# Kernel tuning notes

Measured on AMD Instinct MI355X. Metric: run time of the kernel, lower is better.

The kernel has to match this reference:

```python
import jax, jax.numpy as jnp
import numpy as np

D_MODEL = 1024
NUM_HEADS = 16
D_K = D_MODEL // NUM_HEADS
THETA = 10000.0
BATCH = 2
SEQ = 2048


def setup_inputs() -> dict:
    key = jax.random.key(0)
    ks = jax.random.split(key, 5)
    std = np.sqrt(2.0 / (D_MODEL + D_MODEL))
    return {
        "x": jax.random.normal(ks[0], (BATCH, SEQ, D_MODEL), dtype=jnp.float32),
        "Wq": jax.random.normal(ks[1], (D_MODEL, D_MODEL), dtype=jnp.float32) * std,
        "Wk": jax.random.normal(ks[2], (D_MODEL, D_MODEL), dtype=jnp.float32) * std,
        "Wv": jax.random.normal(ks[3], (D_MODEL, D_MODEL), dtype=jnp.float32) * std,
        "Wo": jax.random.normal(ks[4], (D_MODEL, D_MODEL), dtype=jnp.float32) * std,
        "token_positions": jnp.arange(SEQ, dtype=jnp.int64),
    }


def _apply_rope(t, cos, sin):
    # t: [B, H, S, D_K]; cos/sin: [S, D_K//2]
    # Block-diag 2x2 rotation on consecutive pairs (2k, 2k+1) == elementwise rotation.
    tr = t.reshape(*t.shape[:-1], D_K // 2, 2)
    t0, t1 = tr[..., 0], tr[..., 1]
    o0 = t0 * cos - t1 * sin
    o1 = t0 * sin + t1 * cos
    return jnp.stack([o0, o1], axis=-1).reshape(t.shape)


def reference(x, Wq, Wk, Wv, Wo, token_positions):
    B, S, _ = x.shape
    # projections: custom Linear does x @ W.T
    def split_heads(t):
        return t.reshape(B, S, NUM_HEADS, D_K).transpose(0, 2, 1, 3)  # [B,H,S,Dk]

    q = split_heads(x @ Wq.T)
    k = split_heads(x @ Wk.T)
    v = split_heads(x @ Wv.T)

    # RoPE angle table: theta_ik = pos / THETA**(2k/d_k)
    inv_freq = 1.0 / (THETA ** (2.0 * jnp.arange(D_K // 2, dtype=jnp.float32) / D_K))
    angles = token_positions.astype(jnp.float32)[:, None] * inv_freq[None, :]  # [S, Dk//2]
    cos, sin = jnp.cos(angles), jnp.sin(angles)

    q = _apply_rope(q, cos, sin)
    k = _apply_rope(k, cos, sin)

    scale = 1.0 / np.sqrt(D_K)
    scores = jnp.einsum("bhqd,bhkd->bhqk", q, k) * scale  # [B,H,S,S]
    causal = jnp.tril(jnp.ones((S, S), dtype=bool))
    scores = jnp.where(causal, scores, -jnp.inf)
    attn = jax.nn.softmax(scores, axis=-1)
    out = jnp.einsum("bhqk,bhkd->bhqd", attn, v)  # [B,H,S,Dk]
    out = out.transpose(0, 2, 1, 3).reshape(B, S, D_MODEL)
    return out @ Wo.T
```

## Files before the change

kernel.cpp:

```cpp
#include <hip/hip_runtime.h>
#include <hip/hip_bf16.h>
#include <cstdint>
#include <cstddef>

#define BATCH 2
#define SEQ   2048
#define DM    1024
#define NH    16
#define DK    64
#define LOG2E 1.4426950408889634f

typedef __attribute__((ext_vector_type(8)))  short short8;
typedef __attribute__((ext_vector_type(4)))  float f32x4;
typedef __attribute__((ext_vector_type(16))) float f32x16;
typedef __attribute__((ext_vector_type(4)))  int   i32x4;
typedef __attribute__((ext_vector_type(2)))  int   i32x2;

__device__ __forceinline__ void gload_lds16(const __hip_bfloat16* g, __hip_bfloat16* l) {
  __builtin_amdgcn_global_load_lds((const __attribute__((address_space(1))) void*)g,
                                   (__attribute__((address_space(3))) void*)l, 16, 0, 0);
}

__device__ __forceinline__ int cvtpk_bf16(float lo, float hi) {
  int r;
  asm("v_cvt_pk_bf16_f32 %0, %1, %2" : "=v"(r) : "v"(lo), "v"(hi));
  return r;
}

__device__ __forceinline__ float bf2f(short v) {
  return __int_as_float(((int)(unsigned short)v) << 16);
}

__device__ __forceinline__ float partner32(float x, int hi) {
  auto r = __builtin_amdgcn_permlane32_swap(__float_as_int(x), __float_as_int(x), false, false);
  return __int_as_float(hi ? r[0] : r[1]);
}

__global__ void cast_all(const float* __restrict__ x,  const float* __restrict__ Wq,
                         const float* __restrict__ Wk, const float* __restrict__ Wv,
                         const float* __restrict__ Wo, __hip_bfloat16* __restrict__ dst,
                         const int* __restrict__ pos,  float2* __restrict__ tbl) {
  const int NX = BATCH * SEQ * DM;
  int t = blockIdx.x * 256 + threadIdx.x;
  if (t < SEQ * 32) {
    int s = t >> 5, d2 = t & 31;
    float ang = (float)pos[s] * exp2f(-(float)d2 * 0.415241011860920f);
    float cv, sv;
    __sincosf(ang, &sv, &cv);
    tbl[t] = make_float2(cv, sv);
  }
  size_t i = (size_t)t * 4;
  const float* s;
  if (i < (size_t)NX) {
    s = x + i;
  } else {
    size_t j = i - NX;
    int wsel = (int)(j >> 20);
    size_t o = j & ((1u << 20) - 1);
    s = (wsel == 0 ? Wq : wsel == 1 ? Wk : wsel == 2 ? Wv : Wo) + o;
  }
  float4 v = *(const float4*)s;
  i32x2 pk;
  pk[0] = cvtpk_bf16(v.x, v.y);
  pk[1] = cvtpk_bf16(v.z, v.w);
  *(i32x2*)(dst + i) = pk;
}

template<bool F32OUT, bool VSPLIT>
__global__ __launch_bounds__(256)
void gemm_bt(const __hip_bfloat16* __restrict__ A,
             const __hip_bfloat16* __restrict__ Bw,
             void* __restrict__ Cv, __hip_bfloat16* __restrict__ vt,
             int M, int N, int K, int ldc) {
  __shared__ __hip_bfloat16 As[2][128 * 32];
  __shared__ __hip_bfloat16 Bs[2][128 * 32];
  const int tid  = threadIdx.x;
  const int lane = tid & 63;
  const int w    = tid >> 6;
  const int wr   = w >> 1, wc = w & 1;
  const int g    = lane >> 4;
  const int lr   = lane & 15;

  const int nwg = gridDim.x * gridDim.y;
  const int bid = blockIdx.y * gridDim.x + blockIdx.x;
  const int cpx = nwg >> 3;
  const int sbid = (bid & 7) * cpx + (bid >> 3);
  const int bx = sbid % gridDim.x, by = sbid / gridDim.x;
  const int bm0  = by * 128;
  const int bn0  = bx * 128;

  f32x4 acc[4][4] = {};

  const int strow = lane >> 2;
  const int stcol = (lane & 3) * 8;

  auto STAGE = [&](int buf, int kt) {
    #pragma unroll
    for (int it = 0; it < 2; ++it) {
      int row = (w * 2 + it) * 16 + strow;
      gload_lds16(A  + (size_t)(bm0 + row) * K + kt + stcol, &As[buf][row * 32 + stcol]);
      gload_lds16(Bw + (size_t)(bn0 + row) * K + kt + stcol, &Bs[buf][row * 32 + stcol]);
    }
  };

  STAGE(0, 0);
  __syncthreads();
  int cur = 0;
  const int nk = K / 32;
  for (int ki = 0; ki < nk; ++ki) {
    if (ki + 1 < nk) STAGE(cur ^ 1, (ki + 1) * 32);
    short8 a[4], b[4];
    #pragma unroll
    for (int m = 0; m < 4; ++m)
      a[m] = *(const short8*)(&As[cur][(wr * 64 + m * 16 + lr) * 32 + g * 8]);
    #pragma unroll
    for (int n = 0; n < 4; ++n)
      b[n] = *(const short8*)(&Bs[cur][(wc * 64 + n * 16 + lr) * 32 + g * 8]);
    #pragma unroll
    for (int m = 0; m < 4; ++m)
      #pragma unroll
      for (int n = 0; n < 4; ++n)
        acc[m][n] = __builtin_amdgcn_mfma_f32_16x16x32_bf16(a[m], b[n], acc[m][n], 0, 0, 0);
    __syncthreads();
    cur ^= 1;
  }

  if (VSPLIT && bn0 >= 2048) {
    #pragma unroll
    for (int m = 0; m < 4; ++m)
      #pragma unroll
      for (int n = 0; n < 4; ++n) {
        int nn = bn0 + wc * 64 + n * 16 + lr - 2048;
        int hd = nn >> 6, d = nn & 63;
        int m0 = bm0 + wr * 64 + m * 16 + g * 4;
        int bb = m0 >> 11, ss = m0 & 2047;
        i32x2 pk;
        pk[0] = cvtpk_bf16(acc[m][n][0], acc[m][n][1]);
        pk[1] = cvtpk_bf16(acc[m][n][2], acc[m][n][3]);
        *(i32x2*)(vt + ((size_t)(bb * NH + hd) * DK + d) * SEQ + ss) = pk;
      }
  } else {
    #pragma unroll
    for (int m = 0; m < 4; ++m)
      #pragma unroll
      for (int n = 0; n < 4; ++n) {
        int col = bn0 + wc * 64 + n * 16 + lr;
        #pragma unroll
        for (int r = 0; r < 4; ++r) {
          int row = bm0 + wr * 64 + m * 16 + g * 4 + r;
          float v = acc[m][n][r];
          if (F32OUT) ((float*)Cv)[(size_t)row * ldc + col] = v;
          else        ((__hip_bfloat16*)Cv)[(size_t)row * ldc + col] = __float2bfloat16(v);
        }
      }
  }
}

__global__ void rope_vec(__hip_bfloat16* __restrict__ qk, const float2* __restrict__ tbl) {
  int idx = blockIdx.x * 256 + threadIdx.x;
  int row = idx >> 7;
  int hg  = idx & 127;
  int h   = hg >> 3, gg = hg & 7;
  const float QS = 0.125f * LOG2E;
  size_t base = (size_t)row * 2048 + h * 64 + gg * 8;
  const float2* tp = tbl + (row & (SEQ - 1)) * 32 + gg * 4;
  short8 q = *(const short8*)(qk + base);
  short8 k = *(const short8*)(qk + base + 1024);
  i32x4 qo, ko;
  #pragma unroll
  for (int j = 0; j < 4; ++j) {
    float2 cs = tp[j];
    float q0 = bf2f(q[2 * j]), q1 = bf2f(q[2 * j + 1]);
    float k0 = bf2f(k[2 * j]), k1 = bf2f(k[2 * j + 1]);
    qo[j] = cvtpk_bf16((q0 * cs.x - q1 * cs.y) * QS, (q0 * cs.y + q1 * cs.x) * QS);
    ko[j] = cvtpk_bf16(k0 * cs.x - k1 * cs.y,        k0 * cs.y + k1 * cs.x);
  }
  *(i32x4*)(qk + base)        = qo;
  *(i32x4*)(qk + base + 1024) = ko;
}

__global__ __launch_bounds__(512)
void flash_attn(const __hip_bfloat16* __restrict__ qk,
                const __hip_bfloat16* __restrict__ vt,
                __hip_bfloat16* __restrict__ outb) {
  __shared__ __hip_bfloat16 Kls[2][2][64 * 64];
  __shared__ __hip_bfloat16 Vls[2][2][64 * 64];
  const int pi = blockIdx.x;
  const int NQB = SEQ / 128;
  const int qbh = NQB - 1 - pi, qbl = pi;
  const int hd = blockIdx.y, b = blockIdx.z;
  const int tid = threadIdx.x, lane = tid & 63, w = tid >> 6;
  const int wh = w & 3;
  const int qb_eff = (w < 4) ? qbh : qbl;
  const int hi = lane >> 5, ql = lane & 31;
  const int q0w = qb_eff * 128 + wh * 32;
  const int nph  = qbh + 1;

  const __hip_bfloat16* Qb = qk + (size_t)(b * SEQ) * 2048 + hd * DK;
  const __hip_bfloat16* Kg = qk + (size_t)(b * SEQ) * 2048 + 1024 + hd * DK;
  const __hip_bfloat16* Vg = vt + (size_t)(b * NH + hd) * DK * SEQ;

  short8 qf[4];
  #pragma unroll
  for (int c = 0; c < 4; ++c)
    qf[c] = *(const short8*)(Qb + (size_t)(q0w + ql) * 2048 + c * 16 + hi * 8);

  f32x16 o0 = {}, o1 = {};
  float l_run = 0.f;

  const int srow = tid >> 3;
  const int sc0  = (tid & 7) * 8;
  const int swz  = (srow & 7) << 3;

  short8 kr0, kr1, vr0, vr1;
  auto LOAD = [&](int ph) {
    int r0 = ph * 128;
    kr0 = *(const short8*)(Kg + (size_t)(r0 + srow) * 2048 + sc0);
    kr1 = *(const short8*)(Kg + (size_t)(r0 + 64 + srow) * 2048 + sc0);
    vr0 = *(const short8*)(Vg + (size_t)srow * SEQ + r0 + sc0);
    vr1 = *(const short8*)(Vg + (size_t)srow * SEQ + r0 + 64 + sc0);
  };
  auto WRITE = [&](int buf) {
    *(short8*)(&Kls[buf][0][srow * 64 + (sc0 ^ swz)]) = kr0;
    *(short8*)(&Kls[buf][1][srow * 64 + (sc0 ^ swz)]) = kr1;
    *(short8*)(&Vls[buf][0][srow * 64 + (sc0 ^ swz)]) = vr0;
    *(short8*)(&Vls[buf][1][srow * 64 + (sc0 ^ swz)]) = vr1;
  };

  LOAD(0);
  WRITE(0);

  for (int ph = 0; ph < nph; ++ph) {
    const int cur = ph & 1;
    if (ph + 1 < nph) LOAD(ph + 1);
    __syncthreads();

    if (ph <= qb_eff) {
      const int t0 = 2 * ph, t1 = 2 * ph + 1;

      f32x16 sA0 = {}, sA1 = {}, sB0 = {}, sB1 = {};
      __builtin_amdgcn_s_setprio(1);
      #pragma unroll
      for (int c = 0; c < 4; ++c) {
        int col = (c * 16 + hi * 8) ^ ((ql & 7) << 3);
        short8 ka = *(const short8*)(&Kls[cur][0][ql * 64 + col]);
        short8 kb = *(const short8*)(&Kls[cur][0][(32 + ql) * 64 + col]);
        short8 kc = *(const short8*)(&Kls[cur][1][ql * 64 + col]);
        short8 kd = *(const short8*)(&Kls[cur][1][(32 + ql) * 64 + col]);
        sA0 = __builtin_amdgcn_mfma_f32_32x32x16_bf16(ka, qf[c], sA0, 0, 0, 0);
        sA1 = __builtin_amdgcn_mfma_f32_32x32x16_bf16(kb, qf[c], sA1, 0, 0, 0);
        sB0 = __builtin_amdgcn_mfma_f32_32x32x16_bf16(kc, qf[c], sB0, 0, 0, 0);
        sB1 = __builtin_amdgcn_mfma_f32_32x32x16_bf16(kd, qf[c], sB1, 0, 0, 0);
      }
      __builtin_amdgcn_s_setprio(0);

      if (t0 * 64 + 63 > q0w) {
        int qg = q0w + ql;
        #pragma unroll
        for (int r = 0; r < 16; ++r) {
          int krow = (r & 3) + 8 * (r >> 2) + 4 * hi;
          if (t0 * 64 + krow > qg)      sA0[r] = -1e30f;
          if (t0 * 64 + 32 + krow > qg) sA1[r] = -1e30f;
        }
      }
      if (t1 * 64 + 63 > q0w) {
        int qg = q0w + ql;
        #pragma unroll
        for (int r = 0; r < 16; ++r) {
          int krow = (r & 3) + 8 * (r >> 2) + 4 * hi;
          if (t1 * 64 + krow > qg)      sB0[r] = -1e30f;
          if (t1 * 64 + 32 + krow > qg) sB1[r] = -1e30f;
        }
      }

      float sum = 0.f;
      #pragma unroll
      for (int r = 0; r < 16; ++r) { sA0[r] = __builtin_amdgcn_exp2f(sA0[r]); sum += sA0[r]; }
      #pragma unroll
      for (int r = 0; r < 16; ++r) { sA1[r] = __builtin_amdgcn_exp2f(sA1[r]); sum += sA1[r]; }
      #pragma unroll
      for (int r = 0; r < 16; ++r) { sB0[r] = __builtin_amdgcn_exp2f(sB0[r]); sum += sB0[r]; }
      #pragma unroll
      for (int r = 0; r < 16; ++r) { sB1[r] = __builtin_amdgcn_exp2f(sB1[r]); sum += sB1[r]; }
      sum += partner32(sum, hi);
      l_run += sum;

      short8 pfA[4], pfB[4];
      #pragma unroll
      for (int kt = 0; kt < 2; ++kt) {
        const f32x16& sv = kt ? sA1 : sA0;
        #pragma unroll
        for (int u = 0; u < 2; ++u) {
          int wa0 = cvtpk_bf16(sv[8 * u + 0], sv[8 * u + 1]);
          int wa1 = cvtpk_bf16(sv[8 * u + 2], sv[8 * u + 3]);
          int wb0 = cvtpk_bf16(sv[8 * u + 4], sv[8 * u + 5]);
          int wb1 = cvtpk_bf16(sv[8 * u + 6], sv[8 * u + 7]);
          auto r0 = __builtin_amdgcn_permlane32_swap(wa0, wb0, false, false);
          auto r1 = __builtin_amdgcn_permlane32_swap(wa1, wb1, false, false);
          i32x4 fr; fr[0] = r0[0]; fr[1] = r1[0]; fr[2] = r0[1]; fr[3] = r1[1];
          pfA[kt * 2 + u] = *(short8*)&fr;
        }
      }
      #pragma unroll
      for (int kt = 0; kt < 2; ++kt) {
        const f32x16& sv = kt ? sB1 : sB0;
        #pragma unroll
        for (int u = 0; u < 2; ++u) {
          int wa0 = cvtpk_bf16(sv[8 * u + 0], sv[8 * u + 1]);
          int wa1 = cvtpk_bf16(sv[8 * u + 2], sv[8 * u + 3]);
          int wb0 = cvtpk_bf16(sv[8 * u + 4], sv[8 * u + 5]);
          int wb1 = cvtpk_bf16(sv[8 * u + 6], sv[8 * u + 7]);
          auto r0 = __builtin_amdgcn_permlane32_swap(wa0, wb0, false, false);
          auto r1 = __builtin_amdgcn_permlane32_swap(wa1, wb1, false, false);
          i32x4 fr; fr[0] = r0[0]; fr[1] = r1[0]; fr[2] = r0[1]; fr[3] = r1[1];
          pfB[kt * 2 + u] = *(short8*)&fr;
        }
      }

      __builtin_amdgcn_s_setprio(1);
      #pragma unroll
      for (int cc = 0; cc < 4; ++cc) {
        int col = (cc * 16 + hi * 8) ^ ((ql & 7) << 3);
        short8 va = *(const short8*)(&Vls[cur][0][ql * 64 + col]);
        short8 vb = *(const short8*)(&Vls[cur][0][(32 + ql) * 64 + col]);
        o0 = __builtin_amdgcn_mfma_f32_32x32x16_bf16(va, pfA[cc], o0, 0, 0, 0);
        o1 = __builtin_amdgcn_mfma_f32_32x32x16_bf16(vb, pfA[cc], o1, 0, 0, 0);
      }
      #pragma unroll
      for (int cc = 0; cc < 4; ++cc) {
        int col = (cc * 16 + hi * 8) ^ ((ql & 7) << 3);
        short8 vc = *(const short8*)(&Vls[cur][1][ql * 64 + col]);
        short8 vd = *(const short8*)(&Vls[cur][1][(32 + ql) * 64 + col]);
        o0 = __builtin_amdgcn_mfma_f32_32x32x16_bf16(vc, pfB[cc], o0, 0, 0, 0);
        o1 = __builtin_amdgcn_mfma_f32_32x32x16_bf16(vd, pfB[cc], o1, 0, 0, 0);
      }
      __builtin_amdgcn_s_setprio(0);
    }

    if (ph + 1 < nph) WRITE(cur ^ 1);
  }

  float inv = 1.f / l_run;
  __hip_bfloat16* orow = outb + (size_t)(b * SEQ + q0w + ql) * DM + hd * DK;
  #pragma unroll
  for (int dt = 0; dt < 2; ++dt) {
    const f32x16& oa = dt ? o1 : o0;
    #pragma unroll
    for (int a = 0; a < 4; ++a) {
      int d0 = dt * 32 + a * 8 + hi * 4;
      i32x2 pk;
      pk[0] = cvtpk_bf16(oa[4 * a + 0] * inv, oa[4 * a + 1] * inv);
      pk[1] = cvtpk_bf16(oa[4 * a + 2] * inv, oa[4 * a + 3] * inv);
      *(i32x2*)(orow + d0) = pk;
    }
  }
}

extern "C" void kernel_launch(void* const* d_in, const int* in_sizes, int n_in,
                              void* d_out, int out_size, void* d_ws, size_t ws_size,
                              hipStream_t stream) {
  const float* x  = (const float*)d_in[0];
  const float* Wq = (const float*)d_in[1];
  const float* Wk = (const float*)d_in[2];
  const float* Wv = (const float*)d_in[3];
  const float* Wo = (const float*)d_in[4];
  const int*   tp = (const int*)d_in[5];
  float* out = (float*)d_out;

  char* ws = (char*)d_ws;
  __hip_bfloat16* xb    = (__hip_bfloat16*)(ws);
  __hip_bfloat16* wqkv  = (__hip_bfloat16*)(ws + (8u  << 20));
  __hip_bfloat16* wob   = (__hip_bfloat16*)(ws + (14u << 20));
  __hip_bfloat16* qkbuf = (__hip_bfloat16*)(ws + (16u << 20));
  __hip_bfloat16* vtbuf = (__hip_bfloat16*)(ws + (32u << 20));
  __hip_bfloat16* attnb = (__hip_bfloat16*)(ws + (40u << 20));
  float2*         tbl   = (float2*)(ws + (40u << 20));

  cast_all<<<8192, 256, 0, stream>>>(x, Wq, Wk, Wv, Wo, xb, tp, tbl);

  gemm_bt<false, true><<<dim3(3 * DM / 128, BATCH * SEQ / 128), 256, 0, stream>>>(
      xb, wqkv, (void*)qkbuf, vtbuf, BATCH * SEQ, 3 * DM, DM, 2048);

  rope_vec<<<(BATCH * SEQ * NH * 8) / 256, 256, 0, stream>>>(qkbuf, tbl);

  flash_attn<<<dim3(SEQ / 256, NH, BATCH), 512, 0, stream>>>(qkbuf, vtbuf, attnb);

  gemm_bt<true, false><<<dim3(DM / 128, BATCH * SEQ / 128), 256, 0, stream>>>(
      attnb, wob, (void*)out, nullptr, BATCH * SEQ, DM, DM, DM);
}
```

Measured before the change: 110.0 us.

## Use a dedicated 256x256-tile QKV GEMM with 4-slot LDS pipeline and swizzle

Replaces the generic 128x128 GEMM for the QKV projection with a 512-thread kernel that computes 256x256 tiles. It uses a four-slot LDS ring with two tiles in flight, explicit vmcnt waits instead of full syncthreads, an XOR swizzle to avoid LDS bank conflicts, and raises priority around the MFMA block. The aim is more data reuse per load and better overlap of loads with matrix math. The trade-off is fewer workgroups (192), so fewer CUs get work, plus a much higher register footprint.

```diff
diff --git a/kernel.cpp b/kernel.cpp
--- a/kernel.cpp
+++ b/kernel.cpp
@@ -15,6 +15,11 @@
 typedef __attribute__((ext_vector_type(16))) float f32x16;
 typedef __attribute__((ext_vector_type(4)))  int   i32x4;
 typedef __attribute__((ext_vector_type(2)))  int   i32x2;
+
+#define VM4()     asm volatile("s_waitcnt vmcnt(4)" ::: "memory")
+#define VM0()     asm volatile("s_waitcnt vmcnt(0)" ::: "memory")
+#define BARRIER() do { asm volatile("" ::: "memory"); __builtin_amdgcn_s_barrier(); \
+                       asm volatile("" ::: "memory"); } while (0)
 
 __device__ __forceinline__ void gload_lds16(const __hip_bfloat16* g, __hip_bfloat16* l) {
   __builtin_amdgcn_global_load_lds((const __attribute__((address_space(1))) void*)g,
@@ -66,12 +71,113 @@
   *(i32x2*)(dst + i) = pk;
 }
 
-template<bool F32OUT, bool VSPLIT>
+__global__ __launch_bounds__(512)
+void gemm_qkv_256(const __hip_bfloat16* __restrict__ A,
+                  const __hip_bfloat16* __restrict__ Bw,
+                  __hip_bfloat16* __restrict__ Cqk,
+                  __hip_bfloat16* __restrict__ vt,
+                  int M, int N, int K) {
+  __shared__ __hip_bfloat16 As[4][256 * 32];
+  __shared__ __hip_bfloat16 Bs[4][256 * 32];
+  const int tid  = threadIdx.x;
+  const int lane = tid & 63;
+  const int w    = tid >> 6;
+  const int wm   = w >> 2;
+  const int wn   = w & 3;
+  const int g    = lane >> 4;
+  const int lr   = lane & 15;
+
+  const int nwg = gridDim.x * gridDim.y;
+  const int bid = blockIdx.y * gridDim.x + blockIdx.x;
+  const int cpx = nwg >> 3;
+  const int sbid = (bid & 7) * cpx + (bid >> 3);
+  const int bx = sbid % gridDim.x, by = sbid / gridDim.x;
+  const int bm0 = by * 256, bn0 = bx * 256;
+
+  f32x4 acc[8][4] = {};
+
+  const int strow = tid >> 2;
+  const int stc   = tid & 3;
+
+  auto STAGE = [&](int t) {
+    const int slot = t & 3;
+    const int kt = t * 32;
+    #pragma unroll
+    for (int L = 0; L < 2; ++L) {
+      int row  = L * 128 + strow;
+      int csrc = (stc ^ (row & 3)) * 8;
+      gload_lds16(A  + (size_t)(bm0 + row) * K + kt + csrc, &As[slot][row * 32 + stc * 8]);
+      gload_lds16(Bw + (size_t)(bn0 + row) * K + kt + csrc, &Bs[slot][row * 32 + stc * 8]);
+    }
+  };
+
+  const int nk = K >> 5;
+  STAGE(0);
+  STAGE(1);
+  VM4();
+  BARRIER();
+
+  for (int t = 0; t < nk; ++t) {
+    const int slot = t & 3;
+    if (t + 2 < nk) STAGE(t + 2);
+
+    short8 afr[8], bfr[4];
+    #pragma unroll
+    for (int nr = 0; nr < 4; ++nr) {
+      int row = wn * 64 + nr * 16 + lr;
+      bfr[nr] = *(const short8*)(&Bs[slot][row * 32 + ((g ^ (row & 3)) << 3)]);
+    }
+    #pragma unroll
+    for (int mr = 0; mr < 8; ++mr) {
+      int row = wm * 128 + mr * 16 + lr;
+      afr[mr] = *(const short8*)(&As[slot][row * 32 + ((g ^ (row & 3)) << 3)]);
+    }
+    __builtin_amdgcn_s_setprio(1);
+    #pragma unroll
+    for (int mr = 0; mr < 8; ++mr)
+      #pragma unroll
+      for (int nr = 0; nr < 4; ++nr)
+        acc[mr][nr] = __builtin_amdgcn_mfma_f32_16x16x32_bf16(afr[mr], bfr[nr], acc[mr][nr], 0, 0, 0);
+    __builtin_amdgcn_s_setprio(0);
+
+    if (t + 2 < nk)      { VM4(); BARRIER(); }
+    else if (t + 1 < nk) { VM0(); BARRIER(); }
+  }
+
+  if (bn0 >= 2048) {
+    #pragma unroll
+    for (int mr = 0; mr < 8; ++mr)
+      #pragma unroll
+      for (int nr = 0; nr < 4; ++nr) {
+        int nn = bn0 + wn * 64 + nr * 16 + lr - 2048;
+        int hd = nn >> 6, d = nn & 63;
+        int m0 = bm0 + wm * 128 + mr * 16 + g * 4;
+        int bb = m0 >> 11, ss = m0 & 2047;
+        i32x2 pk;
+        pk[0] = cvtpk_bf16(acc[mr][nr][0], acc[mr][nr][1]);
+        pk[1] = cvtpk_bf16(acc[mr][nr][2], acc[mr][nr][3]);
+        *(i32x2*)(vt + ((size_t)(bb * NH + hd) * DK + d) * SEQ + ss) = pk;
+      }
+  } else {
+    #pragma unroll
+    for (int mr = 0; mr < 8; ++mr)
+      #pragma unroll
+      for (int nr = 0; nr < 4; ++nr) {
+        int col = bn0 + wn * 64 + nr * 16 + lr;
+        #pragma unroll
+        for (int r = 0; r < 4; ++r) {
+          int row = bm0 + wm * 128 + mr * 16 + g * 4 + r;
+          Cqk[(size_t)row * 2048 + col] = __float2bfloat16(acc[mr][nr][r]);
+        }
+      }
+  }
+}
+
+template<bool F32OUT>
 __global__ __launch_bounds__(256)
 void gemm_bt(const __hip_bfloat16* __restrict__ A,
              const __hip_bfloat16* __restrict__ Bw,
-             void* __restrict__ Cv, __hip_bfloat16* __restrict__ vt,
-             int M, int N, int K, int ldc) {
+             void* __restrict__ Cv, int M, int N, int K, int ldc) {
   __shared__ __hip_bfloat16 As[2][128 * 32];
   __shared__ __hip_bfloat16 Bs[2][128 * 32];
   const int tid  = threadIdx.x;
@@ -125,35 +231,19 @@
     cur ^= 1;
   }
 
-  if (VSPLIT && bn0 >= 2048) {
-    #pragma unroll
-    for (int m = 0; m < 4; ++m)
-      #pragma unroll
-      for (int n = 0; n < 4; ++n) {
-        int nn = bn0 + wc * 64 + n * 16 + lr - 2048;
-        int hd = nn >> 6, d = nn & 63;
-        int m0 = bm0 + wr * 64 + m * 16 + g * 4;
-        int bb = m0 >> 11, ss = m0 & 2047;
-        i32x2 pk;
-        pk[0] = cvtpk_bf16(acc[m][n][0], acc[m][n][1]);
-        pk[1] = cvtpk_bf16(acc[m][n][2], acc[m][n][3]);
-        *(i32x2*)(vt + ((size_t)(bb * NH + hd) * DK + d) * SEQ + ss) = pk;
-      }
-  } else {
-    #pragma unroll
-    for (int m = 0; m < 4; ++m)
-      #pragma unroll
-      for (int n = 0; n < 4; ++n) {
-        int col = bn0 + wc * 64 + n * 16 + lr;
-        #pragma unroll
-        for (int r = 0; r < 4; ++r) {
-          int row = bm0 + wr * 64 + m * 16 + g * 4 + r;
-          float v = acc[m][n][r];
-          if (F32OUT) ((float*)Cv)[(size_t)row * ldc + col] = v;
-          else        ((__hip_bfloat16*)Cv)[(size_t)row * ldc + col] = __float2bfloat16(v);
-        }
-      }
-  }
+  #pragma unroll
+  for (int m = 0; m < 4; ++m)
+    #pragma unroll
+    for (int n = 0; n < 4; ++n) {
+      int col = bn0 + wc * 64 + n * 16 + lr;
+      #pragma unroll
+      for (int r = 0; r < 4; ++r) {
+        int row = bm0 + wr * 64 + m * 16 + g * 4 + r;
+        float v = acc[m][n][r];
+        if (F32OUT) ((float*)Cv)[(size_t)row * ldc + col] = v;
+        else        ((__hip_bfloat16*)Cv)[(size_t)row * ldc + col] = __float2bfloat16(v);
+      }
+    }
 }
 
 __global__ void rope_vec(__hip_bfloat16* __restrict__ qk, const float2* __restrict__ tbl) {
@@ -378,13 +468,13 @@
 
   cast_all<<<8192, 256, 0, stream>>>(x, Wq, Wk, Wv, Wo, xb, tp, tbl);
 
-  gemm_bt<false, true><<<dim3(3 * DM / 128, BATCH * SEQ / 128), 256, 0, stream>>>(
-      xb, wqkv, (void*)qkbuf, vtbuf, BATCH * SEQ, 3 * DM, DM, 2048);
+  gemm_qkv_256<<<dim3(3 * DM / 256, BATCH * SEQ / 256), 512, 0, stream>>>(
+      xb, wqkv, qkbuf, vtbuf, BATCH * SEQ, 3 * DM, DM);
 
   rope_vec<<<(BATCH * SEQ * NH * 8) / 256, 256, 0, stream>>>(qkbuf, tbl);
 
   flash_attn<<<dim3(SEQ / 256, NH, BATCH), 512, 0, stream>>>(qkbuf, vtbuf, attnb);
 
-  gemm_bt<true, false><<<dim3(DM / 128, BATCH * SEQ / 128), 256, 0, stream>>>(
-      attnb, wob, (void*)out, nullptr, BATCH * SEQ, DM, DM, DM);
-}
+  gemm_bt<true><<<dim3(DM / 128, BATCH * SEQ / 128), 256, 0, stream>>>(
+      attnb, wob, (void*)out, BATCH * SEQ, DM, DM, DM);
+}
```

New measurement: 123.6 us. 12.3% more time.

## Split flash attention into 256-thread blocks over paired 64-row query chunks

Applied to the files above, without the earlier changes.

The attention kernel now uses 4 waves per block instead of 8. Each block handles a high and a low 64-row query chunk, paired for causal load balance, and the grid doubles to 16x16x2 blocks. Each thread now loads twice as much K/V data per phase, and per-wave causal limits are derived from the 32-row query slice. This aims to raise the number of resident blocks and improve load balance across CUs, at the cost of more global traffic per query, since K/V tiles are shared across fewer waves.

```diff
diff --git a/kernel.cpp b/kernel.cpp
--- a/kernel.cpp
+++ b/kernel.cpp
@@ -179,22 +179,21 @@
   *(i32x4*)(qk + base + 1024) = ko;
 }
 
-__global__ __launch_bounds__(512)
+__global__ __launch_bounds__(256)
 void flash_attn(const __hip_bfloat16* __restrict__ qk,
                 const __hip_bfloat16* __restrict__ vt,
                 __hip_bfloat16* __restrict__ outb) {
   __shared__ __hip_bfloat16 Kls[2][2][64 * 64];
   __shared__ __hip_bfloat16 Vls[2][2][64 * 64];
   const int pi = blockIdx.x;
-  const int NQB = SEQ / 128;
-  const int qbh = NQB - 1 - pi, qbl = pi;
+  const int qch_h = 31 - pi, qch_l = pi;
   const int hd = blockIdx.y, b = blockIdx.z;
   const int tid = threadIdx.x, lane = tid & 63, w = tid >> 6;
-  const int wh = w & 3;
-  const int qb_eff = (w < 4) ? qbh : qbl;
+  const int qch = (w < 2) ? qch_h : qch_l;
   const int hi = lane >> 5, ql = lane & 31;
-  const int q0w = qb_eff * 128 + wh * 32;
-  const int nph  = qbh + 1;
+  const int q0w = qch * 64 + (w & 1) * 32;
+  const int nph = (33 - pi) >> 1;
+  const int tmax_ph = (q0w + 31) >> 7;
 
   const __hip_bfloat16* Qb = qk + (size_t)(b * SEQ) * 2048 + hd * DK;
   const __hip_bfloat16* Kg = qk + (size_t)(b * SEQ) * 2048 + 1024 + hd * DK;
@@ -208,23 +207,31 @@
   f32x16 o0 = {}, o1 = {};
   float l_run = 0.f;
 
-  const int srow = tid >> 3;
-  const int sc0  = (tid & 7) * 8;
+  const int srow = tid >> 2;
+  const int c2   = (tid & 3) * 16;
   const int swz  = (srow & 7) << 3;
 
-  short8 kr0, kr1, vr0, vr1;
+  short8 kr00, kr01, kr10, kr11, vr00, vr01, vr10, vr11;
   auto LOAD = [&](int ph) {
     int r0 = ph * 128;
-    kr0 = *(const short8*)(Kg + (size_t)(r0 + srow) * 2048 + sc0);
-    kr1 = *(const short8*)(Kg + (size_t)(r0 + 64 + srow) * 2048 + sc0);
-    vr0 = *(const short8*)(Vg + (size_t)srow * SEQ + r0 + sc0);
-    vr1 = *(const short8*)(Vg + (size_t)srow * SEQ + r0 + 64 + sc0);
+    kr00 = *(const short8*)(Kg + (size_t)(r0 + srow) * 2048 + c2);
+    kr01 = *(const short8*)(Kg + (size_t)(r0 + srow) * 2048 + c2 + 8);
+    kr10 = *(const short8*)(Kg + (size_t)(r0 + 64 + srow) * 2048 + c2);
+    kr11 = *(const short8*)(Kg + (size_t)(r0 + 64 + srow) * 2048 + c2 + 8);
+    vr00 = *(const short8*)(Vg + (size_t)srow * SEQ + r0 + c2);
+    vr01 = *(const short8*)(Vg + (size_t)srow * SEQ + r0 + c2 + 8);
+    vr10 = *(const short8*)(Vg + (size_t)srow * SEQ + r0 + 64 + c2);
+    vr11 = *(const short8*)(Vg + (size_t)srow * SEQ + r0 + 64 + c2 + 8);
   };
   auto WRITE = [&](int buf) {
-    *(short8*)(&Kls[buf][0][srow * 64 + (sc0 ^ swz)]) = kr0;
-    *(short8*)(&Kls[buf][1][srow * 64 + (sc0 ^ swz)]) = kr1;
-    *(short8*)(&Vls[buf][0][srow * 64 + (sc0 ^ swz)]) = vr0;
-    *(short8*)(&Vls[buf][1][srow * 64 + (sc0 ^ swz)]) = vr1;
+    *(short8*)(&Kls[buf][0][srow * 64 + (c2 ^ swz)])       = kr00;
+    *(short8*)(&Kls[buf][0][srow * 64 + ((c2 + 8) ^ swz)]) = kr01;
+    *(short8*)(&Kls[buf][1][srow * 64 + (c2 ^ swz)])       = kr10;
+    *(short8*)(&Kls[buf][1][srow * 64 + ((c2 + 8) ^ swz)]) = kr11;
+    *(short8*)(&Vls[buf][0][srow * 64 + (c2 ^ swz)])       = vr00;
+    *(short8*)(&Vls[buf][0][srow * 64 + ((c2 + 8) ^ swz)]) = vr01;
+    *(short8*)(&Vls[buf][1][srow * 64 + (c2 ^ swz)])       = vr10;
+    *(short8*)(&Vls[buf][1][srow * 64 + ((c2 + 8) ^ swz)]) = vr11;
   };
 
   LOAD(0);
@@ -235,7 +242,7 @@
     if (ph + 1 < nph) LOAD(ph + 1);
     __syncthreads();
 
-    if (ph <= qb_eff) {
+    if (ph <= tmax_ph) {
       const int t0 = 2 * ph, t1 = 2 * ph + 1;
 
       f32x16 sA0 = {}, sA1 = {}, sB0 = {}, sB1 = {};
@@ -383,7 +390,7 @@
 
   rope_vec<<<(BATCH * SEQ * NH * 8) / 256, 256, 0, stream>>>(qkbuf, tbl);
 
-  flash_attn<<<dim3(SEQ / 256, NH, BATCH), 512, 0, stream>>>(qkbuf, vtbuf, attnb);
+  flash_attn<<<dim3(16, NH, BATCH), 256, 0, stream>>>(qkbuf, vtbuf, attnb);
 
   gemm_bt<true, false><<<dim3(DM / 128, BATCH * SEQ / 128), 256, 0, stream>>>(
       attnb, wob, (void*)out, nullptr, BATCH * SEQ, DM, DM, DM);
```

Measured after the change: 122.4 us. 11.3% more time.
